# Kernel optimization log

Measured on AMD Instinct MI355X. Metric: run time of the kernel, lower is better.

## Reference

```python
import jax, jax.numpy as jnp
import numpy as np

M = 4096      # dictionary_size
D = 64        # feature dim
YD = 4        # output dim (y_dim)
FF = 0.999    # forgetting_factor
REG = 1e-2    # regularisation
JITTER = 1e-10
LS = 8.0      # RBF lengthscale


def rbf(a, b):
    # squared-distance RBF Gram via the ||a||^2 + ||b||^2 - 2ab^T identity
    a2 = jnp.sum(a * a, -1)[:, None]
    b2 = jnp.sum(b * b, -1)[None, :]
    d2 = jnp.maximum(a2 + b2 - 2.0 * (a @ b.T), 0.0)
    return jnp.exp(-d2 / (2.0 * LS * LS))


def setup_inputs() -> dict:
    key = jax.random.key(0)
    ks = jax.random.split(key, 7)
    return {
        'dictionary': jax.random.normal(ks[0], (M, D), jnp.float32),
        'mu': jax.random.normal(ks[1], (YD, M, 1), jnp.float32),
        'sigma': jax.random.normal(ks[2], (M, M), jnp.float32),
        'Q': jax.random.normal(ks[3], (M, M), jnp.float32),
        'x': jax.random.normal(ks[4], (D,), jnp.float32),
        'y': jax.random.normal(ks[5], (YD,), jnp.float32),
        'noise_num': jax.random.uniform(ks[6], (YD, 1, 1), jnp.float32),
        'noise_den': jnp.ones((1,), jnp.float32),
        'time_index': jnp.arange(M, dtype=jnp.float32),
        't': M,
    }


def reference(dictionary, mu, sigma, Q, x, y, noise_num, noise_den, time_index, t):
    alloc = time_index >= 0.0                      # (M,) bool: allocated slots
    y_ = y[:, None, None]                          # (YD,1,1)

    # --- B2P forgetting ---
    Kdd = rbf(dictionary, dictionary) * (alloc[:, None] * alloc[None, :])
    sig = FF * sigma + (1.0 - FF) * Kdd
    mu_f = jnp.sqrt(FF) * mu

    # --- kernel evals for new sample ---
    K_dx = rbf(dictionary, x[None, :]) * alloc[:, None]   # (M,1)
    K_xx = rbf(x[None, :], x[None, :]) + JITTER           # (1,1)

    q_ = Q @ K_dx                                         # (M,1)
    pu = jnp.maximum(K_xx - K_dx.T @ q_, 0.0)             # projection uncertainty (1,1)
    h_ = sig @ q_                                         # (M,1)
    npv = jnp.maximum(pu + q_.T @ h_, 0.0)                # noiseless predictive var (1,1)
    pred_mean = q_.T @ mu_f                               # (YD,1,1) via batched matmul
    pv = REG + npv

    # --- augmented (M+1) state ---
    p_ = jnp.concatenate((h_, npv), axis=-2)              # (M+1,1)
    mu_a = jnp.concatenate((mu_f, pred_mean), axis=-2) + (y_ - pred_mean) / pv * p_
    sig_a = jnp.block([[sig, h_], [h_.T, npv]]) - (p_ @ p_.T) / pv
    p2 = jnp.concatenate((q_, -jnp.ones((1, 1), q_.dtype)), axis=0)
    Q_a = jnp.pad(Q, ((0, 1), (0, 1))) + (p2 @ p2.T) / pu

    nnum = noise_num + FF * (y_ - pred_mean) ** 2 / pv
    nden = noise_den + FF

    # --- pruning criterion ---
    x_alloc = jnp.concatenate((alloc, jnp.ones((1,), bool)))

    def crit_low(_):
        return jnp.concatenate((jnp.ones((M, 1), Q_a.dtype), jnp.zeros((1, 1), Q_a.dtype)))

    def crit_mse(_):
        dq = jnp.where(~x_alloc, jnp.inf, jnp.diag(Q_a))
        errors = Q_a @ mu_a / dq[:, None]                 # (YD,M+1,1)
        return jnp.abs(errors).sum(-3)                    # (M+1,1)

    criterion = jax.lax.cond(pu.squeeze() < JITTER, crit_low, crit_mse, None)
    prune = jnp.argmin(criterion)
    denom = jnp.where(~x_alloc[prune], jnp.inf, Q_a[prune, prune])

    # swap (prune <-> last) permutation, then drop last row/col
    perm = jnp.arange(M + 1)
    perm = jnp.where(perm == prune, M, jnp.where(perm == M, prune, perm))

    Q_r = Q_a[perm, :]                                    # row swap
    Qs = Q_r[:-1, prune]                                  # column `prune` after row swap
    Q_n = Q_r[:, perm][:M, :M] - jnp.outer(Qs, Qs) / denom

    mu_n = mu_a[:, perm, :][:, :M, :]
    sig_n = sig_a[perm, :][:, perm][:M, :M]

    dict_n = dictionary.at[prune].set(x)
    ti_n = time_index.at[prune].set(jnp.asarray(t, time_index.dtype))
    alloc_n = ti_n >= 0.0
    sig_n = (alloc_n[:, None] * alloc_n[None, :]) * sig_n
    mu_n = jnp.where((ti_n < 0.0)[:, None], 0.0, mu_n)

    return (mu_n, sig_n, Q_n, dict_n, ti_n, nnum, nden)
```

## Files before the change

kernel.cpp:

```cpp
#include <hip/hip_runtime.h>
#include <math.h>

#define Mn 4096
#define Dn 64
#define MUA_STRIDE 4104

#define OFF_A2   0
#define OFF_CRIT 0
#define OFF_K    4096
#define OFF_Q    8192
#define OFF_H    12288
#define OFF_MUA  16384
#define OFF_QS   32800
#define OFF_QSD  36896
#define SC_PU    40992
#define SC_INVPU 40993
#define SC_NPV   40994
#define SC_PV    40995
#define SC_INVPV 40996
#define SC_DENOM 40997
#define SC_PRUNE 40998
#define OFF_DICTB 49152

#define O_MU   0
#define O_SIG  16384
#define O_Q    16793600
#define O_DICT 33570816
#define O_TI   33832960
#define O_NNUM 33837056
#define O_NDEN 33837060

typedef __attribute__((ext_vector_type(8))) __bf16 bf16x8;
typedef __attribute__((ext_vector_type(4))) float f32x4;

__device__ __forceinline__ float waveReduceSum(float v) {
#pragma unroll
    for (int o = 32; o > 0; o >>= 1) v += __shfl_down(v, o);
    return v;
}

__device__ __forceinline__ unsigned short f2bf_rne(float f) {
    unsigned u = __float_as_uint(f);
    unsigned r = (u + 0x7FFFu + ((u >> 16) & 1u)) >> 16;
    return (unsigned short)r;
}

__global__ void k1_prep(const float* __restrict__ dict, const float* __restrict__ x,
                        const float* __restrict__ ti, float* __restrict__ ws) {
    int row  = blockIdx.x * 4 + (threadIdx.x >> 6);
    int lane = threadIdx.x & 63;
    float d  = dict[row * Dn + lane];
    float xv = x[lane];
    ((unsigned short*)(ws + OFF_DICTB))[row * Dn + lane] = f2bf_rne(d);
    float a2 = waveReduceSum(d * d);
    float x2 = waveReduceSum(xv * xv);
    float dx = waveReduceSum(d * xv);
    if (lane == 0) {
        ws[OFF_A2 + row] = a2;
        float d2 = fmaxf(a2 + x2 - 2.0f * dx, 0.0f);
        float kv = expf(d2 * (-1.0f / 128.0f));
        ws[OFF_K + row] = (ti[row] >= 0.0f) ? kv : 0.0f;
    }
}

__global__ void k2_q(const float* __restrict__ Q, float* __restrict__ ws) {
    __shared__ float red[4];
    const int row = blockIdx.x;
    const int tid = threadIdx.x;
    const float4* Qr = (const float4*)(Q + (size_t)row * Mn);
    const float4* kv = (const float4*)(ws + OFF_K);
    float s = 0.0f;
#pragma unroll
    for (int it = 0; it < 4; ++it) {
        int u = tid + it * 256;
        float4 a = Qr[u], b = kv[u];
        s += a.x * b.x + a.y * b.y + a.z * b.z + a.w * b.w;
    }
    s = waveReduceSum(s);
    if ((tid & 63) == 0) red[tid >> 6] = s;
    __syncthreads();
    if (tid == 0) {
        ws[OFF_Q + row] = red[0] + red[1] + red[2] + red[3];
        ws[OFF_H + row] = 0.0f;
    }
}

__global__ __launch_bounds__(256) void k3_mfma(
        const float* __restrict__ sigma, const float* __restrict__ ti,
        float* __restrict__ ws, float* __restrict__ out) {
    const int tid  = threadIdx.x;
    const int lane = tid & 63;
    const int w    = tid >> 6;
    const int i0 = blockIdx.y * 128 + (w >> 1) * 64;
    const int j0 = blockIdx.x * 128 + (w & 1) * 64;
    const int lr = lane >> 4;
    const int lc = lane & 15;

    const uint4* db = (const uint4*)(ws + OFF_DICTB);

    bf16x8 bfrag[4][2];
    float a2j[4], qj[4], alj[4];
#pragma unroll
    for (int jt = 0; jt < 4; ++jt) {
        const int col = j0 + jt * 16 + lc;
        bfrag[jt][0] = __builtin_bit_cast(bf16x8, db[col * 8 + lr]);
        bfrag[jt][1] = __builtin_bit_cast(bf16x8, db[col * 8 + 4 + lr]);
        a2j[jt] = ws[OFF_A2 + col];
        qj[jt]  = ws[OFF_Q + col];
        alj[jt] = (ti[col] >= 0.0f) ? 1.0f : 0.0f;
    }

    float hacc[4][4];
#pragma unroll
    for (int it = 0; it < 4; ++it)
#pragma unroll
        for (int i = 0; i < 4; ++i) hacc[it][i] = 0.0f;

#pragma unroll
    for (int it = 0; it < 4; ++it) {
        const int arow = i0 + it * 16 + lc;
        bf16x8 af0 = __builtin_bit_cast(bf16x8, db[arow * 8 + lr]);
        bf16x8 af1 = __builtin_bit_cast(bf16x8, db[arow * 8 + 4 + lr]);
        float a2i[4], ali[4];
#pragma unroll
        for (int i = 0; i < 4; ++i) {
            const int rg = i0 + it * 16 + lr * 4 + i;
            a2i[i] = ws[OFF_A2 + rg];
            ali[i] = (ti[rg] >= 0.0f) ? 1.0f : 0.0f;
        }
#pragma unroll
        for (int jt = 0; jt < 4; ++jt) {
            f32x4 acc = {0.0f, 0.0f, 0.0f, 0.0f};
            acc = __builtin_amdgcn_mfma_f32_16x16x32_bf16(af0, bfrag[jt][0], acc, 0, 0, 0);
            acc = __builtin_amdgcn_mfma_f32_16x16x32_bf16(af1, bfrag[jt][1], acc, 0, 0, 0);
            const int colg = j0 + jt * 16 + lc;
#pragma unroll
            for (int i = 0; i < 4; ++i) {
                const int rg = i0 + it * 16 + lr * 4 + i;
                const size_t off = (size_t)rg * Mn + colg;
                float sv  = sigma[off];
                float d2  = fmaxf(a2i[i] + a2j[jt] - 2.0f * acc[i], 0.0f);
                float kv  = __expf(d2 * (-1.0f / 128.0f)) * ali[i] * alj[jt];
                float res = 0.999f * sv + 0.001f * kv;
                out[O_SIG + off] = res;
                hacc[it][i] += res * qj[jt];
            }
        }
    }

#pragma unroll
    for (int it = 0; it < 4; ++it)
#pragma unroll
        for (int i = 0; i < 4; ++i) {
            float v = hacc[it][i];
            v += __shfl_xor(v, 1);
            v += __shfl_xor(v, 2);
            v += __shfl_xor(v, 4);
            v += __shfl_xor(v, 8);
            if (lc == (it * 4 + i)) {
                atomicAdd(ws + OFF_H + i0 + it * 16 + lr * 4 + i, v);
            }
        }
}

__device__ __forceinline__ float blockReduce1024(float v, float* sred) {
    v = waveReduceSum(v);
    int tid = threadIdx.x;
    __syncthreads();
    if ((tid & 63) == 0) sred[tid >> 6] = v;
    __syncthreads();
    float r = 0.0f;
    if (tid == 0) {
#pragma unroll
        for (int i = 0; i < 16; ++i) r += sred[i];
    }
    return r;
}

__global__ __launch_bounds__(1024) void k4_scalars(
        const float* __restrict__ mu, const float* __restrict__ y,
        const float* __restrict__ nn, const float* __restrict__ nd,
        float* __restrict__ ws, float* __restrict__ out) {
    __shared__ float sred[16];
    __shared__ float sb[8];
    const int tid = threadIdx.x;
    const float* k = ws + OFF_K;
    const float* q = ws + OFF_Q;
    const float* h = ws + OFF_H;
    float kq = 0, qh = 0, p0 = 0, p1 = 0, p2 = 0, p3 = 0;
    for (int i = tid; i < Mn; i += 1024) {
        float qi = q[i];
        kq += k[i] * qi;
        qh += qi * h[i];
        p0 += qi * mu[0 * Mn + i];
        p1 += qi * mu[1 * Mn + i];
        p2 += qi * mu[2 * Mn + i];
        p3 += qi * mu[3 * Mn + i];
    }
    float rkq = blockReduce1024(kq, sred);
    float rqh = blockReduce1024(qh, sred);
    float r0 = blockReduce1024(p0, sred);
    float r1 = blockReduce1024(p1, sred);
    float r2 = blockReduce1024(p2, sred);
    float r3 = blockReduce1024(p3, sred);
    if (tid == 0) {
        const float sf = sqrtf(0.999f);
        float pu  = fmaxf(1.0f - rkq, 0.0f);
        float npv = fmaxf(pu + rqh, 0.0f);
        float pv  = 0.01f + npv;
        ws[SC_PU] = pu;
        ws[SC_INVPU] = 1.0f / pu;
        ws[SC_NPV] = npv;
        ws[SC_PV] = pv;
        ws[SC_INVPV] = 1.0f / pv;
        float pm[4] = {sf * r0, sf * r1, sf * r2, sf * r3};
#pragma unroll
        for (int yd = 0; yd < 4; ++yd) {
            float yv = y[yd];
            float dy = yv - pm[yd];
            float dl = dy / pv;
            sb[yd] = dl;
            ws[OFF_MUA + yd * MUA_STRIDE + Mn] = pm[yd] + dl * npv;
            out[O_NNUM + yd] = nn[yd] + 0.999f * (dy * dy) / pv;
        }
        out[O_NDEN] = nd[0] + 0.999f;
    }
    __syncthreads();
    const float sf = sqrtf(0.999f);
    float d0 = sb[0], d1 = sb[1], d2 = sb[2], d3 = sb[3];
    for (int i = tid; i < Mn; i += 1024) {
        float hi = h[i];
        ws[OFF_MUA + 0 * MUA_STRIDE + i] = sf * mu[0 * Mn + i] + d0 * hi;
        ws[OFF_MUA + 1 * MUA_STRIDE + i] = sf * mu[1 * Mn + i] + d1 * hi;
        ws[OFF_MUA + 2 * MUA_STRIDE + i] = sf * mu[2 * Mn + i] + d2 * hi;
        ws[OFF_MUA + 3 * MUA_STRIDE + i] = sf * mu[3 * Mn + i] + d3 * hi;
    }
}

__global__ __launch_bounds__(256) void k5_crit(const float* __restrict__ Q,
                                               const float* __restrict__ ti,
                                               float* __restrict__ ws) {
    __shared__ float sred[4][4];
    const int row = blockIdx.x;
    const int tid = threadIdx.x;
    const float pu = ws[SC_PU];
    if (pu < 1e-10f) {
        if (tid == 0) ws[OFF_CRIT + row] = (row < Mn) ? 1.0f : 0.0f;
        return;
    }
    const float inv_pu = ws[SC_INVPU];
    const bool rin = (row < Mn);
    const float p2i = rin ? ws[OFF_Q + row] : -1.0f;
    const float4* q4  = (const float4*)(ws + OFF_Q);
    const float4* Qr4 = (const float4*)(Q + (size_t)row * Mn);
    const float* mua = ws + OFF_MUA;
    float n0 = 0, n1 = 0, n2 = 0, n3 = 0;
#pragma unroll
    for (int it = 0; it < 4; ++it) {
        int u = tid + it * 256;
        float4 qv = q4[u];
        float4 base = rin ? Qr4[u] : make_float4(0.f, 0.f, 0.f, 0.f);
        float4 qa;
        qa.x = base.x + p2i * qv.x * inv_pu;
        qa.y = base.y + p2i * qv.y * inv_pu;
        qa.z = base.z + p2i * qv.z * inv_pu;
        qa.w = base.w + p2i * qv.w * inv_pu;
        const float4 m0 = *(const float4*)(mua + 0 * MUA_STRIDE + u * 4);
        const float4 m1 = *(const float4*)(mua + 1 * MUA_STRIDE + u * 4);
        const float4 m2 = *(const float4*)(mua + 2 * MUA_STRIDE + u * 4);
        const float4 m3 = *(const float4*)(mua + 3 * MUA_STRIDE + u * 4);
        n0 += qa.x * m0.x + qa.y * m0.y + qa.z * m0.z + qa.w * m0.w;
        n1 += qa.x * m1.x + qa.y * m1.y + qa.z * m1.z + qa.w * m1.w;
        n2 += qa.x * m2.x + qa.y * m2.y + qa.z * m2.z + qa.w * m2.w;
        n3 += qa.x * m3.x + qa.y * m3.y + qa.z * m3.z + qa.w * m3.w;
    }
    n0 = waveReduceSum(n0);
    n1 = waveReduceSum(n1);
    n2 = waveReduceSum(n2);
    n3 = waveReduceSum(n3);
    if ((tid & 63) == 0) {
        int w = tid >> 6;
        sred[w][0] = n0; sred[w][1] = n1; sred[w][2] = n2; sred[w][3] = n3;
    }
    __syncthreads();
    if (tid == 0) {
        float t0 = 0, t1 = 0, t2 = 0, t3 = 0;
#pragma unroll
        for (int w = 0; w < 4; ++w) {
            t0 += sred[w][0]; t1 += sred[w][1]; t2 += sred[w][2]; t3 += sred[w][3];
        }
        float qaM = -p2i * inv_pu;
        t0 += qaM * mua[0 * MUA_STRIDE + Mn];
        t1 += qaM * mua[1 * MUA_STRIDE + Mn];
        t2 += qaM * mua[2 * MUA_STRIDE + Mn];
        t3 += qaM * mua[3 * MUA_STRIDE + Mn];
        bool xa = rin ? (ti[row] >= 0.0f) : true;
        float crit = 0.0f;
        if (xa) {
            float dq = rin ? (Q[(size_t)row * Mn + row] + p2i * p2i * inv_pu) : inv_pu;
            crit = fabsf(t0 / dq) + fabsf(t1 / dq) + fabsf(t2 / dq) + fabsf(t3 / dq);
        }
        ws[OFF_CRIT + row] = crit;
    }
}

__global__ __launch_bounds__(1024) void k6_argmin(const float* __restrict__ Q,
                                                  const float* __restrict__ ti,
                                                  float* __restrict__ ws) {
    __shared__ float sval[1024];
    __shared__ int   sidx[1024];
    const int tid = threadIdx.x;
    float bv = INFINITY;
    int bi = Mn + 1;
    for (int i = tid; i <= Mn; i += 1024) {
        float v = ws[OFF_CRIT + i];
        if (v < bv) { bv = v; bi = i; }
    }
    sval[tid] = bv; sidx[tid] = bi;
    __syncthreads();
    for (int s = 512; s > 0; s >>= 1) {
        if (tid < s) {
            float ov = sval[tid + s]; int oi = sidx[tid + s];
            if (ov < sval[tid] || (ov == sval[tid] && oi < sidx[tid])) {
                sval[tid] = ov; sidx[tid] = oi;
            }
        }
        __syncthreads();
    }
    if (tid == 0) {
        int prune = sidx[0];
        ((int*)ws)[SC_PRUNE] = prune;
        float inv_pu = ws[SC_INVPU];
        bool xa = (prune == Mn) ? true : (ti[prune] >= 0.0f);
        float qap;
        if (prune < Mn) {
            float qp = ws[OFF_Q + prune];
            qap = Q[(size_t)prune * Mn + prune] + qp * qp * inv_pu;
        } else {
            qap = inv_pu;
        }
        ws[SC_DENOM] = xa ? qap : INFINITY;
    }
}

__global__ void k6b_vec(const float* __restrict__ Q, const float* __restrict__ dict,
                        const float* __restrict__ x, const float* __restrict__ ti,
                        const int* __restrict__ tptr, float* __restrict__ ws,
                        float* __restrict__ out) {
    const int tid = blockIdx.x * 256 + threadIdx.x;
    const int prune = ((const int*)ws)[SC_PRUNE];
    const int row = tid >> 6, col = tid & 63;
    out[O_DICT + tid] = (row == prune) ? x[col] : dict[tid];
    if (tid < Mn) {
        float tv = ti[tid];
        if (tid == prune) {
            int raw = *tptr;
            tv = (raw >= 0 && raw < (1 << 30)) ? (float)raw : __int_as_float(raw);
        }
        out[O_TI + tid] = tv;
        const float inv_pu = ws[SC_INVPU];
        const float denom  = ws[SC_DENOM];
        const float p2p = (prune < Mn) ? ws[OFF_Q + prune] : -1.0f;
        float qs;
        if (tid == prune) {
            qs = -p2p * inv_pu;
        } else {
            float base = (prune < Mn) ? Q[(size_t)tid * Mn + prune] : 0.0f;
            qs = base + ws[OFF_Q + tid] * p2p * inv_pu;
        }
        ws[OFF_QS + tid] = qs;
        ws[OFF_QSD + tid] = qs / denom;
    }
}

__global__ __launch_bounds__(256) void k7_fused(const float* __restrict__ Q,
                                                float* __restrict__ out,
                                                const float* __restrict__ ws) {
    const int i = blockIdx.x;
    const int tid = threadIdx.x;
    const int prune = ((const int*)ws)[SC_PRUNE];
    const float inv_pu = ws[SC_INVPU];
    const float inv_pv = ws[SC_INVPV];
    const float npv = ws[SC_NPV];

    const int pi = (i == prune) ? Mn : i;
    const bool piok = (pi < Mn);
    const float p2i = piok ? ws[OFF_Q + pi] : -1.0f;
    const float qsi = ws[OFF_QS + i];
    const float4* Qr4  = (const float4*)(Q + (size_t)pi * Mn);
    const float4* q4   = (const float4*)(ws + OFF_Q);
    const float4* qsd4 = (const float4*)(ws + OFF_QSD);
    float4* o4 = (float4*)(out + O_Q + (size_t)i * Mn);
#pragma unroll
    for (int it = 0; it < 4; ++it) {
        int u = tid + it * 256;
        float4 base = piok ? Qr4[u] : make_float4(0.f, 0.f, 0.f, 0.f);
        float4 p2j = q4[u];
        if ((prune >> 2) == u) {
            int c = prune & 3;
            ((float*)&p2j)[c] = -1.0f;
            ((float*)&base)[c] = 0.0f;
        }
        float4 d = qsd4[u];
        float4 r;
        r.x = base.x + p2i * p2j.x * inv_pu - qsi * d.x;
        r.y = base.y + p2i * p2j.y * inv_pu - qsi * d.y;
        r.z = base.z + p2i * p2j.z * inv_pu - qsi * d.z;
        r.w = base.w + p2i * p2j.w * inv_pu - qsi * d.w;
        o4[u] = r;
    }

    const bool ip = (i == prune);
    const float ai = (out[O_TI + i] >= 0.0f) ? 1.0f : 0.0f;
    const float hi = ws[OFF_H + i];
    const float p_i = ip ? npv : hi;
    const float4* h4  = (const float4*)(ws + OFF_H);
    const float4* ti4 = (const float4*)(out + O_TI);
    float4* s4 = (float4*)(out + O_SIG + (size_t)i * Mn);
#pragma unroll
    for (int it = 0; it < 4; ++it) {
        int u = tid + it * 256;
        float4 sv = s4[u];
        float4 hj = h4[u];
        float4 tv = ti4[u];
        float pj[4] = {hj.x, hj.y, hj.z, hj.w};
        float bs[4];
        if (ip) { bs[0] = hj.x; bs[1] = hj.y; bs[2] = hj.z; bs[3] = hj.w; }
        else    { bs[0] = sv.x; bs[1] = sv.y; bs[2] = sv.z; bs[3] = sv.w; }
        if ((prune >> 2) == u) {
            int c = prune & 3;
            pj[c] = npv;
            bs[c] = ip ? npv : hi;
        }
        float aj[4] = {tv.x >= 0.f ? 1.f : 0.f, tv.y >= 0.f ? 1.f : 0.f,
                       tv.z >= 0.f ? 1.f : 0.f, tv.w >= 0.f ? 1.f : 0.f};
        float4 r;
        r.x = ai * aj[0] * (bs[0] - p_i * pj[0] * inv_pv);
        r.y = ai * aj[1] * (bs[1] - p_i * pj[1] * inv_pv);
        r.z = ai * aj[2] * (bs[2] - p_i * pj[2] * inv_pv);
        r.w = ai * aj[3] * (bs[3] - p_i * pj[3] * inv_pv);
        s4[u] = r;
    }

    if (tid < 4) {
        float tin = out[O_TI + i];
        float v;
        if (tin < 0.0f) v = 0.0f;
        else v = ws[OFF_MUA + tid * MUA_STRIDE + (ip ? Mn : i)];
        out[O_MU + tid * Mn + i] = v;
    }
}

extern "C" void kernel_launch(void* const* d_in, const int* in_sizes, int n_in,
                              void* d_out, int out_size, void* d_ws, size_t ws_size,
                              hipStream_t stream) {
    const float* dict  = (const float*)d_in[0];
    const float* mu    = (const float*)d_in[1];
    const float* sigma = (const float*)d_in[2];
    const float* Q     = (const float*)d_in[3];
    const float* x     = (const float*)d_in[4];
    const float* y     = (const float*)d_in[5];
    const float* nn    = (const float*)d_in[6];
    const float* nd    = (const float*)d_in[7];
    const float* ti    = (const float*)d_in[8];
    const int*   tptr  = (const int*)d_in[9];
    float* out = (float*)d_out;
    float* ws  = (float*)d_ws;

    k1_prep<<<1024, 256, 0, stream>>>(dict, x, ti, ws);
    k2_q<<<4096, 256, 0, stream>>>(Q, ws);
    k3_mfma<<<dim3(32, 32), 256, 0, stream>>>(sigma, ti, ws, out);
    k4_scalars<<<1, 1024, 0, stream>>>(mu, y, nn, nd, ws, out);
    k5_crit<<<4097, 256, 0, stream>>>(Q, ti, ws);
    k6_argmin<<<1, 1024, 0, stream>>>(Q, ti, ws);
    k6b_vec<<<1024, 256, 0, stream>>>(Q, dict, x, ti, tptr, ws, out);
    k7_fused<<<4096, 256, 0, stream>>>(Q, out, ws);
}
```

Before: 340.2 us.

## Defer sigma write, compute h by GEMV plus kernel term, recompute Gram in final pass

k3 no longer writes the forgotten sigma to the output. It computes h as 0.999*sigma@q through a streaming GEMV, plus a separate MFMA pass that adds only the 0.001*Kdd@q term. The final kernel recomputes the RBF Gram tile with MFMA, reads sigma directly, and applies the rank-one sigma update and the allocation masks in one write. This removes one full 64MB write and one read of the sigma output, at the cost of recomputing the Gram matrix twice and reading sigma twice.

```diff
diff --git a/kernel.cpp b/kernel.cpp
--- a/kernel.cpp
+++ b/kernel.cpp
@@ -85,42 +85,54 @@
     }
 }
 
-__global__ __launch_bounds__(256) void k3_mfma(
+__global__ __launch_bounds__(256) void k3_h(
         const float* __restrict__ sigma, const float* __restrict__ ti,
-        float* __restrict__ ws, float* __restrict__ out) {
+        float* __restrict__ ws) {
     const int tid  = threadIdx.x;
     const int lane = tid & 63;
     const int w    = tid >> 6;
-    const int i0 = blockIdx.y * 128 + (w >> 1) * 64;
-    const int j0 = blockIdx.x * 128 + (w & 1) * 64;
+
+    if (blockIdx.x < 1024) {
+        const int row = blockIdx.x * 4 + w;
+        const float4* S  = (const float4*)(sigma + (size_t)row * Mn);
+        const float4* q4 = (const float4*)(ws + OFF_Q);
+        float s = 0.0f;
+#pragma unroll
+        for (int it = 0; it < 16; ++it) {
+            int u = lane + it * 64;
+            float4 a = S[u], b = q4[u];
+            s += a.x * b.x + a.y * b.y + a.z * b.z + a.w * b.w;
+        }
+        s = waveReduceSum(s);
+        if (lane == 0) atomicAdd(ws + OFF_H + row, 0.999f * s);
+        return;
+    }
+
+    const int t  = blockIdx.x - 1024;
+    const int i0 = (t >> 5) * 128 + (w >> 1) * 64;
+    const int j0 = (t & 31) * 128 + (w & 1) * 64;
     const int lr = lane >> 4;
     const int lc = lane & 15;
-
     const uint4* db = (const uint4*)(ws + OFF_DICTB);
 
     bf16x8 bfrag[4][2];
-    float a2j[4], qj[4], alj[4];
+    float a2j[4], qmj[4];
 #pragma unroll
     for (int jt = 0; jt < 4; ++jt) {
         const int col = j0 + jt * 16 + lc;
         bfrag[jt][0] = __builtin_bit_cast(bf16x8, db[col * 8 + lr]);
         bfrag[jt][1] = __builtin_bit_cast(bf16x8, db[col * 8 + 4 + lr]);
         a2j[jt] = ws[OFF_A2 + col];
-        qj[jt]  = ws[OFF_Q + col];
-        alj[jt] = (ti[col] >= 0.0f) ? 1.0f : 0.0f;
-    }
-
-    float hacc[4][4];
-#pragma unroll
-    for (int it = 0; it < 4; ++it)
-#pragma unroll
-        for (int i = 0; i < 4; ++i) hacc[it][i] = 0.0f;
+        float alj = (ti[col] >= 0.0f) ? 1.0f : 0.0f;
+        qmj[jt] = 0.001f * alj * ws[OFF_Q + col];
+    }
 
 #pragma unroll
     for (int it = 0; it < 4; ++it) {
         const int arow = i0 + it * 16 + lc;
         bf16x8 af0 = __builtin_bit_cast(bf16x8, db[arow * 8 + lr]);
         bf16x8 af1 = __builtin_bit_cast(bf16x8, db[arow * 8 + 4 + lr]);
+        float hacc[4] = {0.f, 0.f, 0.f, 0.f};
         float a2i[4], ali[4];
 #pragma unroll
         for (int i = 0; i < 4; ++i) {
@@ -133,34 +145,23 @@
             f32x4 acc = {0.0f, 0.0f, 0.0f, 0.0f};
             acc = __builtin_amdgcn_mfma_f32_16x16x32_bf16(af0, bfrag[jt][0], acc, 0, 0, 0);
             acc = __builtin_amdgcn_mfma_f32_16x16x32_bf16(af1, bfrag[jt][1], acc, 0, 0, 0);
-            const int colg = j0 + jt * 16 + lc;
 #pragma unroll
             for (int i = 0; i < 4; ++i) {
-                const int rg = i0 + it * 16 + lr * 4 + i;
-                const size_t off = (size_t)rg * Mn + colg;
-                float sv  = sigma[off];
-                float d2  = fmaxf(a2i[i] + a2j[jt] - 2.0f * acc[i], 0.0f);
-                float kv  = __expf(d2 * (-1.0f / 128.0f)) * ali[i] * alj[jt];
-                float res = 0.999f * sv + 0.001f * kv;
-                out[O_SIG + off] = res;
-                hacc[it][i] += res * qj[jt];
+                float d2 = fmaxf(a2i[i] + a2j[jt] - 2.0f * acc[i], 0.0f);
+                float kv = __expf(d2 * (-1.0f / 128.0f)) * ali[i];
+                hacc[i] = fmaf(kv, qmj[jt], hacc[i]);
             }
         }
-    }
-
-#pragma unroll
-    for (int it = 0; it < 4; ++it)
 #pragma unroll
         for (int i = 0; i < 4; ++i) {
-            float v = hacc[it][i];
+            float v = hacc[i];
             v += __shfl_xor(v, 1);
             v += __shfl_xor(v, 2);
             v += __shfl_xor(v, 4);
             v += __shfl_xor(v, 8);
-            if (lc == (it * 4 + i)) {
-                atomicAdd(ws + OFF_H + i0 + it * 16 + lr * 4 + i, v);
-            }
-        }
+            if (lc == i) atomicAdd(ws + OFF_H + i0 + it * 16 + lr * 4 + i, v);
+        }
+    }
 }
 
 __device__ __forceinline__ float blockReduce1024(float v, float* sred) {
@@ -374,80 +375,116 @@
 }
 
 __global__ __launch_bounds__(256) void k7_fused(const float* __restrict__ Q,
+                                                const float* __restrict__ sigma,
+                                                const float* __restrict__ ti,
                                                 float* __restrict__ out,
                                                 const float* __restrict__ ws) {
-    const int i = blockIdx.x;
     const int tid = threadIdx.x;
     const int prune = ((const int*)ws)[SC_PRUNE];
     const float inv_pu = ws[SC_INVPU];
     const float inv_pv = ws[SC_INVPV];
     const float npv = ws[SC_NPV];
 
-    const int pi = (i == prune) ? Mn : i;
-    const bool piok = (pi < Mn);
-    const float p2i = piok ? ws[OFF_Q + pi] : -1.0f;
-    const float qsi = ws[OFF_QS + i];
-    const float4* Qr4  = (const float4*)(Q + (size_t)pi * Mn);
-    const float4* q4   = (const float4*)(ws + OFF_Q);
-    const float4* qsd4 = (const float4*)(ws + OFF_QSD);
-    float4* o4 = (float4*)(out + O_Q + (size_t)i * Mn);
+    if (blockIdx.x < 4096) {
+        const int i = blockIdx.x;
+        const int pi = (i == prune) ? Mn : i;
+        const bool piok = (pi < Mn);
+        const float p2i = piok ? ws[OFF_Q + pi] : -1.0f;
+        const float qsi = ws[OFF_QS + i];
+        const float4* Qr4  = (const float4*)(Q + (size_t)pi * Mn);
+        const float4* q4   = (const float4*)(ws + OFF_Q);
+        const float4* qsd4 = (const float4*)(ws + OFF_QSD);
+        float4* o4 = (float4*)(out + O_Q + (size_t)i * Mn);
+#pragma unroll
+        for (int it = 0; it < 4; ++it) {
+            int u = tid + it * 256;
+            float4 base = piok ? Qr4[u] : make_float4(0.f, 0.f, 0.f, 0.f);
+            float4 p2j = q4[u];
+            if ((prune >> 2) == u) {
+                int c = prune & 3;
+                ((float*)&p2j)[c] = -1.0f;
+                ((float*)&base)[c] = 0.0f;
+            }
+            float4 d = qsd4[u];
+            float4 r;
+            r.x = base.x + p2i * p2j.x * inv_pu - qsi * d.x;
+            r.y = base.y + p2i * p2j.y * inv_pu - qsi * d.y;
+            r.z = base.z + p2i * p2j.z * inv_pu - qsi * d.z;
+            r.w = base.w + p2i * p2j.w * inv_pu - qsi * d.w;
+            o4[u] = r;
+        }
+        if (tid < 4) {
+            float tin = out[O_TI + i];
+            float v;
+            if (tin < 0.0f) v = 0.0f;
+            else v = ws[OFF_MUA + tid * MUA_STRIDE + ((i == prune) ? Mn : i)];
+            out[O_MU + tid * Mn + i] = v;
+        }
+        return;
+    }
+
+    const int t    = blockIdx.x - 4096;
+    const int lane = tid & 63;
+    const int w    = tid >> 6;
+    const int i0 = (t >> 5) * 128 + (w >> 1) * 64;
+    const int j0 = (t & 31) * 128 + (w & 1) * 64;
+    const int lr = lane >> 4;
+    const int lc = lane & 15;
+    const uint4* db = (const uint4*)(ws + OFF_DICTB);
+
+    bf16x8 bfrag[4][2];
+    float a2j[4], hj[4], aljo[4], ajn[4];
+    bool pcol[4];
+#pragma unroll
+    for (int jt = 0; jt < 4; ++jt) {
+        const int col = j0 + jt * 16 + lc;
+        bfrag[jt][0] = __builtin_bit_cast(bf16x8, db[col * 8 + lr]);
+        bfrag[jt][1] = __builtin_bit_cast(bf16x8, db[col * 8 + 4 + lr]);
+        a2j[jt]  = ws[OFF_A2 + col];
+        hj[jt]   = ws[OFF_H + col];
+        aljo[jt] = (ti[col] >= 0.0f) ? 1.0f : 0.0f;
+        ajn[jt]  = (out[O_TI + col] >= 0.0f) ? 1.0f : 0.0f;
+        pcol[jt] = (col == prune);
+    }
+
 #pragma unroll
     for (int it = 0; it < 4; ++it) {
-        int u = tid + it * 256;
-        float4 base = piok ? Qr4[u] : make_float4(0.f, 0.f, 0.f, 0.f);
-        float4 p2j = q4[u];
-        if ((prune >> 2) == u) {
-            int c = prune & 3;
-            ((float*)&p2j)[c] = -1.0f;
-            ((float*)&base)[c] = 0.0f;
-        }
-        float4 d = qsd4[u];
-        float4 r;
-        r.x = base.x + p2i * p2j.x * inv_pu - qsi * d.x;
-        r.y = base.y + p2i * p2j.y * inv_pu - qsi * d.y;
-        r.z = base.z + p2i * p2j.z * inv_pu - qsi * d.z;
-        r.w = base.w + p2i * p2j.w * inv_pu - qsi * d.w;
-        o4[u] = r;
-    }
-
-    const bool ip = (i == prune);
-    const float ai = (out[O_TI + i] >= 0.0f) ? 1.0f : 0.0f;
-    const float hi = ws[OFF_H + i];
-    const float p_i = ip ? npv : hi;
-    const float4* h4  = (const float4*)(ws + OFF_H);
-    const float4* ti4 = (const float4*)(out + O_TI);
-    float4* s4 = (float4*)(out + O_SIG + (size_t)i * Mn);
-#pragma unroll
-    for (int it = 0; it < 4; ++it) {
-        int u = tid + it * 256;
-        float4 sv = s4[u];
-        float4 hj = h4[u];
-        float4 tv = ti4[u];
-        float pj[4] = {hj.x, hj.y, hj.z, hj.w};
-        float bs[4];
-        if (ip) { bs[0] = hj.x; bs[1] = hj.y; bs[2] = hj.z; bs[3] = hj.w; }
-        else    { bs[0] = sv.x; bs[1] = sv.y; bs[2] = sv.z; bs[3] = sv.w; }
-        if ((prune >> 2) == u) {
-            int c = prune & 3;
-            pj[c] = npv;
-            bs[c] = ip ? npv : hi;
-        }
-        float aj[4] = {tv.x >= 0.f ? 1.f : 0.f, tv.y >= 0.f ? 1.f : 0.f,
-                       tv.z >= 0.f ? 1.f : 0.f, tv.w >= 0.f ? 1.f : 0.f};
-        float4 r;
-        r.x = ai * aj[0] * (bs[0] - p_i * pj[0] * inv_pv);
-        r.y = ai * aj[1] * (bs[1] - p_i * pj[1] * inv_pv);
-        r.z = ai * aj[2] * (bs[2] - p_i * pj[2] * inv_pv);
-        r.w = ai * aj[3] * (bs[3] - p_i * pj[3] * inv_pv);
-        s4[u] = r;
-    }
-
-    if (tid < 4) {
-        float tin = out[O_TI + i];
-        float v;
-        if (tin < 0.0f) v = 0.0f;
-        else v = ws[OFF_MUA + tid * MUA_STRIDE + (ip ? Mn : i)];
-        out[O_MU + tid * Mn + i] = v;
+        const int arow = i0 + it * 16 + lc;
+        bf16x8 af0 = __builtin_bit_cast(bf16x8, db[arow * 8 + lr]);
+        bf16x8 af1 = __builtin_bit_cast(bf16x8, db[arow * 8 + 4 + lr]);
+        float a2i[4], alio[4], ain[4], hr[4];
+        bool prow[4];
+#pragma unroll
+        for (int i = 0; i < 4; ++i) {
+            const int rg = i0 + it * 16 + lr * 4 + i;
+            a2i[i]  = ws[OFF_A2 + rg];
+            alio[i] = (ti[rg] >= 0.0f) ? 1.0f : 0.0f;
+            ain[i]  = (out[O_TI + rg] >= 0.0f) ? 1.0f : 0.0f;
+            hr[i]   = ws[OFF_H + rg];
+            prow[i] = (rg == prune);
+        }
+#pragma unroll
+        for (int jt = 0; jt < 4; ++jt) {
+            f32x4 acc = {0.0f, 0.0f, 0.0f, 0.0f};
+            acc = __builtin_amdgcn_mfma_f32_16x16x32_bf16(af0, bfrag[jt][0], acc, 0, 0, 0);
+            acc = __builtin_amdgcn_mfma_f32_16x16x32_bf16(af1, bfrag[jt][1], acc, 0, 0, 0);
+            const int colg = j0 + jt * 16 + lc;
+#pragma unroll
+            for (int i = 0; i < 4; ++i) {
+                const int rg = i0 + it * 16 + lr * 4 + i;
+                const size_t off = (size_t)rg * Mn + colg;
+                float sv = sigma[off];
+                float d2 = fmaxf(a2i[i] + a2j[jt] - 2.0f * acc[i], 0.0f);
+                float kv = __expf(d2 * (-1.0f / 128.0f)) * alio[i] * aljo[jt];
+                float bs = 0.999f * sv + 0.001f * kv;
+                if (pcol[jt]) bs = prow[i] ? npv : hr[i];
+                if (prow[i])  bs = pcol[jt] ? npv : hj[jt];
+                float p_i = prow[i]  ? npv : hr[i];
+                float p_j = pcol[jt] ? npv : hj[jt];
+                float r = ain[i] * ajn[jt] * (bs - p_i * p_j * inv_pv);
+                out[O_SIG + off] = r;
+            }
+        }
     }
 }
 
@@ -469,10 +506,10 @@
 
     k1_prep<<<1024, 256, 0, stream>>>(dict, x, ti, ws);
     k2_q<<<4096, 256, 0, stream>>>(Q, ws);
-    k3_mfma<<<dim3(32, 32), 256, 0, stream>>>(sigma, ti, ws, out);
+    k3_h<<<2048, 256, 0, stream>>>(sigma, ti, ws);
     k4_scalars<<<1, 1024, 0, stream>>>(mu, y, nn, nd, ws, out);
     k5_crit<<<4097, 256, 0, stream>>>(Q, ti, ws);
     k6_argmin<<<1, 1024, 0, stream>>>(Q, ti, ws);
     k6b_vec<<<1024, 256, 0, stream>>>(Q, dict, x, ti, tptr, ws, out);
-    k7_fused<<<4096, 256, 0, stream>>>(Q, out, ws);
-}
+    k7_fused<<<5120, 256, 0, stream>>>(Q, sigma, ti, out, ws);
+}
```

New measurement: 369.3 us. 8.6% more time.
